# Kernel optimization log

Hardware: AMD Instinct MI355X
Metric: run time of the kernel (lower is better)

The kernel has to match this reference:

```python
import jax, jax.numpy as jnp
import numpy as np

DIM = 1024
HEADS = 16
DIM_HEAD = 64
INNER = HEADS * DIM_HEAD  # 1024
SCALE = DIM_HEAD ** -0.5


def setup_inputs() -> dict:
    key = jax.random.key(0)
    ks = jax.random.split(key, 5)
    B, N = 4, 2048
    x = jax.random.normal(ks[0], (B, N, DIM), dtype=jnp.float32)
    # torch Linear weights are [out, in]; store transposed [in, out] for x @ W
    s = 1.0 / np.sqrt(DIM)
    Wq = jax.random.uniform(ks[1], (DIM, INNER), minval=-s, maxval=s, dtype=jnp.float32)
    Wkv = jax.random.uniform(ks[2], (DIM, 2 * INNER), minval=-s, maxval=s, dtype=jnp.float32)
    so = 1.0 / np.sqrt(INNER)
    Wo = jax.random.uniform(ks[3], (INNER, DIM), minval=-so, maxval=so, dtype=jnp.float32)
    bo = jax.random.uniform(ks[4], (DIM,), minval=-so, maxval=so, dtype=jnp.float32)
    return {"x": x, "Wq": Wq, "Wkv": Wkv, "Wo": Wo, "bo": bo}


def reference(x, Wq, Wkv, Wo, bo):
    B, N, _ = x.shape
    q = x @ Wq                      # [B, N, INNER]
    kv = x @ Wkv                    # [B, N, 2*INNER]
    k, v = jnp.split(kv, 2, axis=-1)

    def split_heads(t):
        return t.reshape(B, N, HEADS, DIM_HEAD).transpose(0, 2, 1, 3)  # [B,H,N,D]

    q, k, v = split_heads(q) * SCALE, split_heads(k), split_heads(v)
    sim = jnp.einsum('bhid,bhjd->bhij', q, k)  # [B,H,N,N]
    mask_value = -jnp.finfo(sim.dtype).max
    # causal: mask strictly-upper triangle (triu with offset j-i+1 = 1)
    causal_mask = jnp.triu(jnp.ones((N, N), dtype=bool), k=1)
    sim = jnp.where(causal_mask[None, None, :, :], mask_value, sim)
    attn = jax.nn.softmax(sim, axis=-1)
    out = jnp.einsum('bhij,bhjd->bhid', attn, v)            # [B,H,N,D]
    out = out.transpose(0, 2, 1, 3).reshape(B, N, INNER)    # [B,N,INNER]
    return out @ Wo + bo
```

## Files before the change

kernel.cpp:

```cpp
#include <hip/hip_runtime.h>

typedef unsigned short u16;
typedef __bf16 bf16x8 __attribute__((ext_vector_type(8)));
typedef float floatx4 __attribute__((ext_vector_type(4)));
typedef unsigned as1_u32 __attribute__((address_space(1)));
typedef unsigned as3_u32 __attribute__((address_space(3)));

__device__ inline u16 f2bf(float f) {
    unsigned int u = __builtin_bit_cast(unsigned int, f);
    u += 0x7fffu + ((u >> 16) & 1u);
    return (u16)(u >> 16);
}
__device__ inline floatx4 mfma16(bf16x8 a, bf16x8 b, floatx4 c) {
    return __builtin_amdgcn_mfma_f32_16x16x32_bf16(a, b, c, 0, 0, 0);
}
__device__ inline void gld16(const u16* g, u16* l) {
    __builtin_amdgcn_global_load_lds((const as1_u32*)g, (as3_u32*)l, 16, 0, 0);
}
__device__ inline unsigned permpack(float lo, float hi) {
    return __builtin_amdgcn_perm(__builtin_bit_cast(unsigned, hi),
                                 __builtin_bit_cast(unsigned, lo), 0x07060302u);
}

#define NSEQ 2048
#define DIM  1024
#define HEADS 16
#define DHEAD 64
#define QSCALE 0.18033688f
#define CSHIFT 4.328085f

__global__ __launch_bounds__(256) void conv_x(const float* __restrict__ src,
                                              u16* __restrict__ dst) {
    const size_t i = ((size_t)blockIdx.x * 256 + threadIdx.x) * 8;
    float4 a = *(const float4*)&src[i];
    float4 b = *(const float4*)&src[i + 4];
    u16 o[8] __attribute__((aligned(16)));
    o[0] = f2bf(a.x); o[1] = f2bf(a.y); o[2] = f2bf(a.z); o[3] = f2bf(a.w);
    o[4] = f2bf(b.x); o[5] = f2bf(b.y); o[6] = f2bf(b.z); o[7] = f2bf(b.w);
    *(uint4*)&dst[i] = *(const uint4*)o;
}

__global__ __launch_bounds__(256) void transpose_conv(const float* __restrict__ src,
                                                      u16* __restrict__ dst, int ncols) {
    __shared__ u16 tile[64][72];
    const int n0 = blockIdx.x * 64, k0 = blockIdx.y * 64;
    const int t = threadIdx.x;
    #pragma unroll
    for (int rr = 0; rr < 4; rr++) {
        const int k = (t >> 4) + rr * 16;
        const int n = (t & 15) * 4;
        float4 v = *(const float4*)&src[(size_t)(k0 + k) * ncols + n0 + n];
        tile[n + 0][k] = f2bf(v.x); tile[n + 1][k] = f2bf(v.y);
        tile[n + 2][k] = f2bf(v.z); tile[n + 3][k] = f2bf(v.w);
    }
    __syncthreads();
    #pragma unroll
    for (int ww = 0; ww < 2; ww++) {
        const int idx = t + ww * 256;
        const int n = idx >> 3, g = idx & 7;
        u16 tmp[8] __attribute__((aligned(16)));
        #pragma unroll
        for (int i = 0; i < 8; i++) tmp[i] = tile[n][g * 8 + i];
        *(uint4*)&dst[(size_t)(n0 + n) * 1024 + k0 + g * 8] = *(const uint4*)tmp;
    }
}

__global__ __launch_bounds__(256) void qkv_gemm_v3(
    const u16* __restrict__ xb, const u16* __restrict__ Wt,
    u16* __restrict__ q_ws, u16* __restrict__ k_ws, u16* __restrict__ v_ws)
{
    __shared__ u16 a0[128 * 32], a1[128 * 32];
    __shared__ u16 b0[128 * 32], b1[128 * 32];

    const int n0 = blockIdx.x * 128;
    const int m0 = blockIdx.y * 128;
    const int t = threadIdx.x, lane = t & 63, w = t >> 6;
    const int wr = w >> 1, wc = w & 1;
    const int quad = lane >> 4, l16 = lane & 15;
    const int lrow = lane >> 2, lk = (lane & 3) * 8;

    floatx4 acc[4][4];
    #pragma unroll
    for (int i = 0; i < 4; i++)
        #pragma unroll
        for (int j = 0; j < 4; j++) acc[i][j] = floatx4{0.f, 0.f, 0.f, 0.f};

    for (int k0 = 0; k0 < DIM; k0 += 64) {
        __syncthreads();
        #pragma unroll
        for (int hh = 0; hh < 2; hh++) {
            const int row = w * 32 + hh * 16;
            const size_t ga = (size_t)(m0 + row + lrow) * DIM + k0 + lk;
            const size_t gb = (size_t)(n0 + row + lrow) * DIM + k0 + lk;
            gld16(&xb[ga],      &a0[row * 32]);
            gld16(&xb[ga + 32], &a1[row * 32]);
            gld16(&Wt[gb],      &b0[row * 32]);
            gld16(&Wt[gb + 32], &b1[row * 32]);
        }
        __syncthreads();

        #pragma unroll
        for (int ks = 0; ks < 2; ks++) {
            const u16* al = ks ? a1 : a0;
            const u16* bl = ks ? b1 : b0;
            bf16x8 af[4], bf[4];
            #pragma unroll
            for (int i = 0; i < 4; i++)
                af[i] = *(const bf16x8*)&al[(wr * 64 + i * 16 + l16) * 32 + quad * 8];
            #pragma unroll
            for (int j = 0; j < 4; j++)
                bf[j] = *(const bf16x8*)&bl[(wc * 64 + j * 16 + l16) * 32 + quad * 8];
            #pragma unroll
            for (int i = 0; i < 4; i++)
                #pragma unroll
                for (int j = 0; j < 4; j++)
                    acc[i][j] = mfma16(af[i], bf[j], acc[i][j]);
        }
    }

    const int seg = n0 >> 10;
    #pragma unroll
    for (int j = 0; j < 4; j++) {
        const int n  = n0 + wc * 64 + j * 16 + l16;
        const int nn = n & 1023;
        const int h  = nn >> 6, d = nn & 63;
        #pragma unroll
        for (int i = 0; i < 4; i++) {
            const int mb = m0 + wr * 64 + i * 16 + quad * 4;
            const int b = mb >> 11, ib = mb & (NSEQ - 1);
            if (seg == 0) {
                #pragma unroll
                for (int r = 0; r < 4; r++)
                    q_ws[(((size_t)(b * HEADS + h)) * NSEQ + ib + r) * DHEAD + d] =
                        f2bf(acc[i][j][r] * QSCALE);
            } else if (seg == 1) {
                #pragma unroll
                for (int r = 0; r < 4; r++)
                    k_ws[(((size_t)(b * HEADS + h)) * NSEQ + ib + r) * DHEAD + d] =
                        f2bf(acc[i][j][r]);
            } else {
                u16 tmp[4] __attribute__((aligned(8)));
                #pragma unroll
                for (int r = 0; r < 4; r++) tmp[r] = f2bf(acc[i][j][r]);
                *(uint2*)&v_ws[(((size_t)(b * HEADS + h)) * DHEAD + d) * NSEQ + ib] =
                    *(const uint2*)tmp;
            }
        }
    }
}

__global__ __launch_bounds__(256) void attn_v6(
    const u16* __restrict__ q_ws, const u16* __restrict__ k_ws,
    const u16* __restrict__ v_ws, u16* __restrict__ attn_ws)
{
    __shared__ u16 kds[2][64 * 64];
    __shared__ u16 vds[2][64 * 64];
    __shared__ u16 p_lds[4 * 32 * 72];

    const int bid = blockIdx.x;
    const int bh  = bid & 63;
    const int t16 = 15 - (bid >> 6);
    const int i0  = t16 * 128;
    const int b   = bh >> 4, h = bh & 15;

    const u16* qb = q_ws + (size_t)bh * NSEQ * DHEAD;
    const u16* kb = k_ws + (size_t)bh * NSEQ * DHEAD;
    const u16* vb = v_ws + (size_t)bh * DHEAD * NSEQ;

    const int t    = threadIdx.x;
    const int lane = t & 63, w = t >> 6;
    const int quad = lane >> 4, l16 = lane & 15;

    const int srow8 = lane >> 3;
    const int chunk = (lane & 7) ^ srow8;
    const int krow  = w * 16 + srow8;
    const size_t koff = (size_t)krow * DHEAD + chunk * 8;
    const size_t voff = (size_t)krow * NSEQ + chunk * 8;
    u16* klbase = (u16*)&kds[0][0] + w * 1024;
    u16* vlbase = (u16*)&vds[0][0] + w * 1024;

    bf16x8 qf[2][2];
    #pragma unroll
    for (int rf = 0; rf < 2; rf++)
        #pragma unroll
        for (int dg = 0; dg < 2; dg++)
            qf[rf][dg] = *(const bf16x8*)&qb[(size_t)(i0 + rf * 64 + w * 16 + l16) * DHEAD
                                             + dg * 32 + quad * 8];

    floatx4 l4[2] = {floatx4{0.f,0.f,0.f,0.f}, floatx4{0.f,0.f,0.f,0.f}};
    floatx4 acc[2][4];
    #pragma unroll
    for (int rf = 0; rf < 2; rf++)
        #pragma unroll
        for (int dg = 0; dg < 4; dg++) acc[rf][dg] = floatx4{0.f, 0.f, 0.f, 0.f};

    const int jt_max = 2 * t16 + 1;

    {
        gld16(&kb[koff],               klbase);
        gld16(&kb[koff + 8 * DHEAD],   klbase + 512);
        gld16(&vb[voff],               vlbase);
        gld16(&vb[voff + 8 * NSEQ],    vlbase + 512);
    }

    for (int jt = 0; jt <= jt_max; jt++) {
        const int cur = jt & 1;
        __syncthreads();

        if (jt < jt_max) {
            const size_t j64 = (size_t)(jt + 1) * 64;
            const int nb = (cur ^ 1) * 4096;
            gld16(&kb[j64 * DHEAD + koff],             klbase + nb);
            gld16(&kb[j64 * DHEAD + koff + 8 * DHEAD], klbase + nb + 512);
            gld16(&vb[j64 + voff],                     vlbase + nb);
            gld16(&vb[j64 + voff + 8 * NSEQ],          vlbase + nb + 512);
        }

        const u16* kl = &kds[cur][0];
        const u16* vl = &vds[cur][0];
        const int j0 = jt * 64;
        const int sw = (l16 & 7);

        floatx4 s[2][4];
        #pragma unroll
        for (int rf = 0; rf < 2; rf++)
            #pragma unroll
            for (int g = 0; g < 4; g++)
                s[rf][g] = floatx4{-CSHIFT, -CSHIFT, -CSHIFT, -CSHIFT};
        #pragma unroll
        for (int dg = 0; dg < 2; dg++)
            #pragma unroll
            for (int g = 0; g < 4; g++) {
                bf16x8 kf = *(const bf16x8*)&kl[(g * 16 + l16) * 64
                                                + (((dg * 4 + quad) ^ sw) * 8)];
                s[0][g] = mfma16(kf, qf[0][dg], s[0][g]);
                s[1][g] = mfma16(kf, qf[1][dg], s[1][g]);
            }

        #pragma unroll
        for (int rf = 0; rf < 2; rf++) {
            const int imin = i0 + rf * 64 + w * 16;
            if (j0 + 63 > imin) {
                const int i = imin + l16;
                #pragma unroll
                for (int g = 0; g < 4; g++) {
                    const int jb = j0 + g * 16 + quad * 4;
                    #pragma unroll
                    for (int r = 0; r < 4; r++)
                        if (jb + r > i) s[rf][g][r] = -1e30f;
                }
            }
        }

        #pragma unroll
        for (int rf = 0; rf < 2; rf++) {
            #pragma unroll
            for (int g = 0; g < 4; g++) {
                #pragma unroll
                for (int r = 0; r < 4; r++)
                    s[rf][g][r] = __builtin_amdgcn_exp2f(s[rf][g][r]);
                l4[rf] += s[rf][g];
                uint2 pk;
                pk.x = permpack(s[rf][g][0], s[rf][g][1]);
                pk.y = permpack(s[rf][g][2], s[rf][g][3]);
                *(uint2*)&p_lds[w * 2304 + (rf * 16 + l16) * 72 + g * 16 + quad * 4] = pk;
            }
        }
        asm volatile("s_waitcnt lgkmcnt(0)" ::: "memory");

        #pragma unroll
        for (int jg = 0; jg < 2; jg++) {
            bf16x8 pf0 = *(const bf16x8*)&p_lds[w * 2304 + l16 * 72 + jg * 32 + quad * 8];
            bf16x8 pf1 = *(const bf16x8*)&p_lds[w * 2304 + (16 + l16) * 72 + jg * 32 + quad * 8];
            #pragma unroll
            for (int dg = 0; dg < 4; dg++) {
                bf16x8 vf = *(const bf16x8*)&vl[(dg * 16 + l16) * 64
                                                + (((jg * 4 + quad) ^ sw) * 8)];
                acc[0][dg] = mfma16(pf0, vf, acc[0][dg]);
                acc[1][dg] = mfma16(pf1, vf, acc[1][dg]);
            }
        }
    }

    float l_ln[2];
    #pragma unroll
    for (int rf = 0; rf < 2; rf++) {
        l_ln[rf] = (l4[rf][0] + l4[rf][1]) + (l4[rf][2] + l4[rf][3]);
        l_ln[rf] += __shfl_xor(l_ln[rf], 16);
        l_ln[rf] += __shfl_xor(l_ln[rf], 32);
    }

    #pragma unroll
    for (int rf = 0; rf < 2; rf++) {
        float l_row[4];
        #pragma unroll
        for (int r = 0; r < 4; r++)
            l_row[r] = __shfl(l_ln[rf], quad * 4 + r);
        #pragma unroll
        for (int dg = 0; dg < 4; dg++)
            #pragma unroll
            for (int r = 0; r < 4; r++) {
                const float o = acc[rf][dg][r] / l_row[r];
                const int i = i0 + rf * 64 + w * 16 + quad * 4 + r;
                attn_ws[(((size_t)(b * NSEQ + i)) * HEADS + h) * DHEAD + dg * 16 + l16] = f2bf(o);
            }
    }
}

__global__ __launch_bounds__(256) void out_gemm_v3(
    const u16* __restrict__ attn, const u16* __restrict__ Wot,
    const float* __restrict__ bo, float* __restrict__ out)
{
    __shared__ u16 a0[128 * 32], a1[128 * 32];
    __shared__ u16 b0[128 * 32], b1[128 * 32];

    const int n0 = blockIdx.x * 128;
    const int m0 = blockIdx.y * 128;
    const int t = threadIdx.x, lane = t & 63, w = t >> 6;
    const int wr = w >> 1, wc = w & 1;
    const int quad = lane >> 4, l16 = lane & 15;
    const int lrow = lane >> 2, lk = (lane & 3) * 8;

    floatx4 acc[4][4];
    #pragma unroll
    for (int i = 0; i < 4; i++)
        #pragma unroll
        for (int j = 0; j < 4; j++) acc[i][j] = floatx4{0.f, 0.f, 0.f, 0.f};

    for (int k0 = 0; k0 < DIM; k0 += 64) {
        __syncthreads();
        #pragma unroll
        for (int hh = 0; hh < 2; hh++) {
            const int row = w * 32 + hh * 16;
            const size_t ga = (size_t)(m0 + row + lrow) * DIM + k0 + lk;
            const size_t gb = (size_t)(n0 + row + lrow) * DIM + k0 + lk;
            gld16(&attn[ga],      &a0[row * 32]);
            gld16(&attn[ga + 32], &a1[row * 32]);
            gld16(&Wot[gb],       &b0[row * 32]);
            gld16(&Wot[gb + 32],  &b1[row * 32]);
        }
        __syncthreads();

        #pragma unroll
        for (int ks = 0; ks < 2; ks++) {
            const u16* al = ks ? a1 : a0;
            const u16* bl = ks ? b1 : b0;
            bf16x8 af[4], bf[4];
            #pragma unroll
            for (int i = 0; i < 4; i++)
                af[i] = *(const bf16x8*)&al[(wr * 64 + i * 16 + l16) * 32 + quad * 8];
            #pragma unroll
            for (int j = 0; j < 4; j++)
                bf[j] = *(const bf16x8*)&bl[(wc * 64 + j * 16 + l16) * 32 + quad * 8];
            #pragma unroll
            for (int i = 0; i < 4; i++)
                #pragma unroll
                for (int j = 0; j < 4; j++)
                    acc[i][j] = mfma16(af[i], bf[j], acc[i][j]);
        }
    }

    #pragma unroll
    for (int j = 0; j < 4; j++) {
        const int n = n0 + wc * 64 + j * 16 + l16;
        const float bias = bo[n];
        #pragma unroll
        for (int i = 0; i < 4; i++) {
            #pragma unroll
            for (int r = 0; r < 4; r++) {
                const int m = m0 + wr * 64 + i * 16 + quad * 4 + r;
                out[(size_t)m * DIM + n] = acc[i][j][r] + bias;
            }
        }
    }
}

extern "C" void kernel_launch(void* const* d_in, const int* in_sizes, int n_in,
                              void* d_out, int out_size, void* d_ws, size_t ws_size,
                              hipStream_t stream) {
    const float* x   = (const float*)d_in[0];
    const float* Wq  = (const float*)d_in[1];
    const float* Wkv = (const float*)d_in[2];
    const float* Wo  = (const float*)d_in[3];
    const float* bo  = (const float*)d_in[4];

    u16* q_ws = (u16*)d_out;
    u16* xb   = (u16*)d_out + (size_t)8388608;

    u16* ws   = (u16*)d_ws;
    u16* k_ws = ws;
    u16* v_ws = ws + (size_t)8388608;
    u16* a_ws = ws + (size_t)16777216;
    u16* Wt   = a_ws;
    u16* Wot  = k_ws;

    conv_x<<<4096, 256, 0, stream>>>(x, xb);
    transpose_conv<<<dim3(16, 16), 256, 0, stream>>>(Wq, Wt, 1024);
    transpose_conv<<<dim3(32, 16), 256, 0, stream>>>(Wkv, Wt + (size_t)1024 * 1024, 2048);
    qkv_gemm_v3<<<dim3(24, 64), 256, 0, stream>>>(xb, Wt, q_ws, k_ws, v_ws);
    attn_v6<<<dim3(1024), 256, 0, stream>>>(q_ws, k_ws, v_ws, a_ws);
    transpose_conv<<<dim3(16, 16), 256, 0, stream>>>(Wo, Wot, 1024);
    out_gemm_v3<<<dim3(8, 64), 256, 0, stream>>>(a_ws, Wot, bo, (float*)d_out);
}
```

Baseline: 256.8 us.

## Enlarge QKV GEMM tile to 256x128 and pair causal attention tiles per block

The QKV GEMM now uses a 256x128 output tile with each wave owning 64 rows across all 128 columns, which doubles B-fragment reuse per wave and halves the grid. The attention kernel now processes two query tiles per block, a long one (15-pr) and a short one (pr), so every block does the same amount of causal work and the grid is 512 blocks. The GEMM change raises accumulator register use (4x8 floatx4) and may lower occupancy. Halving the attention grid reduces parallelism on a many-CU device.

```diff
diff --git a/kernel.cpp b/kernel.cpp
--- a/kernel.cpp
+++ b/kernel.cpp
@@ -65,35 +65,38 @@
     }
 }
 
-__global__ __launch_bounds__(256) void qkv_gemm_v3(
+__global__ __launch_bounds__(256) void qkv_gemm_v4(
     const u16* __restrict__ xb, const u16* __restrict__ Wt,
     u16* __restrict__ q_ws, u16* __restrict__ k_ws, u16* __restrict__ v_ws)
 {
-    __shared__ u16 a0[128 * 32], a1[128 * 32];
+    __shared__ u16 a0[256 * 32], a1[256 * 32];
     __shared__ u16 b0[128 * 32], b1[128 * 32];
 
     const int n0 = blockIdx.x * 128;
-    const int m0 = blockIdx.y * 128;
+    const int m0 = blockIdx.y * 256;
     const int t = threadIdx.x, lane = t & 63, w = t >> 6;
-    const int wr = w >> 1, wc = w & 1;
     const int quad = lane >> 4, l16 = lane & 15;
     const int lrow = lane >> 2, lk = (lane & 3) * 8;
 
-    floatx4 acc[4][4];
+    floatx4 acc[4][8];
     #pragma unroll
     for (int i = 0; i < 4; i++)
         #pragma unroll
-        for (int j = 0; j < 4; j++) acc[i][j] = floatx4{0.f, 0.f, 0.f, 0.f};
+        for (int j = 0; j < 8; j++) acc[i][j] = floatx4{0.f, 0.f, 0.f, 0.f};
 
     for (int k0 = 0; k0 < DIM; k0 += 64) {
         __syncthreads();
         #pragma unroll
+        for (int hh = 0; hh < 4; hh++) {
+            const int row = w * 64 + hh * 16;
+            const size_t ga = (size_t)(m0 + row + lrow) * DIM + k0 + lk;
+            gld16(&xb[ga],      &a0[row * 32]);
+            gld16(&xb[ga + 32], &a1[row * 32]);
+        }
+        #pragma unroll
         for (int hh = 0; hh < 2; hh++) {
             const int row = w * 32 + hh * 16;
-            const size_t ga = (size_t)(m0 + row + lrow) * DIM + k0 + lk;
             const size_t gb = (size_t)(n0 + row + lrow) * DIM + k0 + lk;
-            gld16(&xb[ga],      &a0[row * 32]);
-            gld16(&xb[ga + 32], &a1[row * 32]);
             gld16(&Wt[gb],      &b0[row * 32]);
             gld16(&Wt[gb + 32], &b1[row * 32]);
         }
@@ -103,30 +106,30 @@
         for (int ks = 0; ks < 2; ks++) {
             const u16* al = ks ? a1 : a0;
             const u16* bl = ks ? b1 : b0;
-            bf16x8 af[4], bf[4];
+            bf16x8 af[4], bf[8];
             #pragma unroll
             for (int i = 0; i < 4; i++)
-                af[i] = *(const bf16x8*)&al[(wr * 64 + i * 16 + l16) * 32 + quad * 8];
-            #pragma unroll
-            for (int j = 0; j < 4; j++)
-                bf[j] = *(const bf16x8*)&bl[(wc * 64 + j * 16 + l16) * 32 + quad * 8];
+                af[i] = *(const bf16x8*)&al[(w * 64 + i * 16 + l16) * 32 + quad * 8];
+            #pragma unroll
+            for (int j = 0; j < 8; j++)
+                bf[j] = *(const bf16x8*)&bl[(j * 16 + l16) * 32 + quad * 8];
             #pragma unroll
             for (int i = 0; i < 4; i++)
                 #pragma unroll
-                for (int j = 0; j < 4; j++)
+                for (int j = 0; j < 8; j++)
                     acc[i][j] = mfma16(af[i], bf[j], acc[i][j]);
         }
     }
 
     const int seg = n0 >> 10;
     #pragma unroll
-    for (int j = 0; j < 4; j++) {
-        const int n  = n0 + wc * 64 + j * 16 + l16;
+    for (int j = 0; j < 8; j++) {
+        const int n  = n0 + j * 16 + l16;
         const int nn = n & 1023;
         const int h  = nn >> 6, d = nn & 63;
         #pragma unroll
         for (int i = 0; i < 4; i++) {
-            const int mb = m0 + wr * 64 + i * 16 + quad * 4;
+            const int mb = m0 + w * 64 + i * 16 + quad * 4;
             const int b = mb >> 11, ib = mb & (NSEQ - 1);
             if (seg == 0) {
                 #pragma unroll
@@ -149,7 +152,7 @@
     }
 }
 
-__global__ __launch_bounds__(256) void attn_v6(
+__global__ __launch_bounds__(256) void attn_v7(
     const u16* __restrict__ q_ws, const u16* __restrict__ k_ws,
     const u16* __restrict__ v_ws, u16* __restrict__ attn_ws)
 {
@@ -159,8 +162,7 @@
 
     const int bid = blockIdx.x;
     const int bh  = bid & 63;
-    const int t16 = 15 - (bid >> 6);
-    const int i0  = t16 * 128;
+    const int pr  = bid >> 6;
     const int b   = bh >> 4, h = bh & 15;
 
     const u16* qb = q_ws + (size_t)bh * NSEQ * DHEAD;
@@ -178,132 +180,130 @@
     const size_t voff = (size_t)krow * NSEQ + chunk * 8;
     u16* klbase = (u16*)&kds[0][0] + w * 1024;
     u16* vlbase = (u16*)&vds[0][0] + w * 1024;
-
-    bf16x8 qf[2][2];
-    #pragma unroll
-    for (int rf = 0; rf < 2; rf++)
-        #pragma unroll
-        for (int dg = 0; dg < 2; dg++)
-            qf[rf][dg] = *(const bf16x8*)&qb[(size_t)(i0 + rf * 64 + w * 16 + l16) * DHEAD
-                                             + dg * 32 + quad * 8];
-
-    floatx4 l4[2] = {floatx4{0.f,0.f,0.f,0.f}, floatx4{0.f,0.f,0.f,0.f}};
-    floatx4 acc[2][4];
-    #pragma unroll
-    for (int rf = 0; rf < 2; rf++)
-        #pragma unroll
-        for (int dg = 0; dg < 4; dg++) acc[rf][dg] = floatx4{0.f, 0.f, 0.f, 0.f};
-
-    const int jt_max = 2 * t16 + 1;
-
-    {
-        gld16(&kb[koff],               klbase);
-        gld16(&kb[koff + 8 * DHEAD],   klbase + 512);
-        gld16(&vb[voff],               vlbase);
-        gld16(&vb[voff + 8 * NSEQ],    vlbase + 512);
-    }
-
-    for (int jt = 0; jt <= jt_max; jt++) {
-        const int cur = jt & 1;
-        __syncthreads();
-
-        if (jt < jt_max) {
-            const size_t j64 = (size_t)(jt + 1) * 64;
-            const int nb = (cur ^ 1) * 4096;
-            gld16(&kb[j64 * DHEAD + koff],             klbase + nb);
-            gld16(&kb[j64 * DHEAD + koff + 8 * DHEAD], klbase + nb + 512);
-            gld16(&vb[j64 + voff],                     vlbase + nb);
-            gld16(&vb[j64 + voff + 8 * NSEQ],          vlbase + nb + 512);
-        }
-
-        const u16* kl = &kds[cur][0];
-        const u16* vl = &vds[cur][0];
-        const int j0 = jt * 64;
-        const int sw = (l16 & 7);
-
-        floatx4 s[2][4];
+    const int sw = (l16 & 7);
+
+    for (int ph = 0; ph < 2; ph++) {
+        const int t16 = ph ? pr : (15 - pr);
+        const int i0  = t16 * 128;
+        const int jt_max = 2 * t16 + 1;
+
+        bf16x8 qf[2][2];
         #pragma unroll
         for (int rf = 0; rf < 2; rf++)
             #pragma unroll
-            for (int g = 0; g < 4; g++)
-                s[rf][g] = floatx4{-CSHIFT, -CSHIFT, -CSHIFT, -CSHIFT};
-        #pragma unroll
-        for (int dg = 0; dg < 2; dg++)
-            #pragma unroll
-            for (int g = 0; g < 4; g++) {
-                bf16x8 kf = *(const bf16x8*)&kl[(g * 16 + l16) * 64
-                                                + (((dg * 4 + quad) ^ sw) * 8)];
-                s[0][g] = mfma16(kf, qf[0][dg], s[0][g]);
-                s[1][g] = mfma16(kf, qf[1][dg], s[1][g]);
-            }
-
-        #pragma unroll
-        for (int rf = 0; rf < 2; rf++) {
-            const int imin = i0 + rf * 64 + w * 16;
-            if (j0 + 63 > imin) {
-                const int i = imin + l16;
+            for (int dg = 0; dg < 2; dg++)
+                qf[rf][dg] = *(const bf16x8*)&qb[(size_t)(i0 + rf * 64 + w * 16 + l16) * DHEAD
+                                                 + dg * 32 + quad * 8];
+
+        floatx4 l4[2] = {floatx4{0.f,0.f,0.f,0.f}, floatx4{0.f,0.f,0.f,0.f}};
+        floatx4 acc[2][4];
+        #pragma unroll
+        for (int rf = 0; rf < 2; rf++)
+            #pragma unroll
+            for (int dg = 0; dg < 4; dg++) acc[rf][dg] = floatx4{0.f, 0.f, 0.f, 0.f};
+
+        gld16(&kb[koff],             klbase);
+        gld16(&kb[koff + 8 * DHEAD], klbase + 512);
+        gld16(&vb[voff],             vlbase);
+        gld16(&vb[voff + 8 * NSEQ],  vlbase + 512);
+
+        for (int jt = 0; jt <= jt_max; jt++) {
+            const int cur = jt & 1;
+            __syncthreads();
+
+            if (jt < jt_max) {
+                const size_t j64 = (size_t)(jt + 1) * 64;
+                const int nb = (cur ^ 1) * 4096;
+                gld16(&kb[j64 * DHEAD + koff],             klbase + nb);
+                gld16(&kb[j64 * DHEAD + koff + 8 * DHEAD], klbase + nb + 512);
+                gld16(&vb[j64 + voff],                     vlbase + nb);
+                gld16(&vb[j64 + voff + 8 * NSEQ],          vlbase + nb + 512);
+            }
+
+            const u16* kl = &kds[cur][0];
+            const u16* vl = &vds[cur][0];
+            const int j0 = jt * 64;
+
+            floatx4 s[2][4];
+            #pragma unroll
+            for (int rf = 0; rf < 2; rf++)
+                #pragma unroll
+                for (int g = 0; g < 4; g++)
+                    s[rf][g] = floatx4{-CSHIFT, -CSHIFT, -CSHIFT, -CSHIFT};
+            #pragma unroll
+            for (int dg = 0; dg < 2; dg++)
                 #pragma unroll
                 for (int g = 0; g < 4; g++) {
-                    const int jb = j0 + g * 16 + quad * 4;
+                    bf16x8 kf = *(const bf16x8*)&kl[(g * 16 + l16) * 64
+                                                    + (((dg * 4 + quad) ^ sw) * 8)];
+                    s[0][g] = mfma16(kf, qf[0][dg], s[0][g]);
+                    s[1][g] = mfma16(kf, qf[1][dg], s[1][g]);
+                }
+
+            #pragma unroll
+            for (int rf = 0; rf < 2; rf++) {
+                const int imin = i0 + rf * 64 + w * 16;
+                if (j0 + 63 > imin) {
+                    const int i = imin + l16;
+                    #pragma unroll
+                    for (int g = 0; g < 4; g++) {
+                        const int jb = j0 + g * 16 + quad * 4;
+                        #pragma unroll
+                        for (int r = 0; r < 4; r++)
+                            if (jb + r > i) s[rf][g][r] = -1e30f;
+                    }
+                }
+            }
+
+            #pragma unroll
+            for (int rf = 0; rf < 2; rf++) {
+                #pragma unroll
+                for (int g = 0; g < 4; g++) {
                     #pragma unroll
                     for (int r = 0; r < 4; r++)
-                        if (jb + r > i) s[rf][g][r] = -1e30f;
+                        s[rf][g][r] = __builtin_amdgcn_exp2f(s[rf][g][r]);
+                    l4[rf] += s[rf][g];
+                    uint2 pk;
+                    pk.x = permpack(s[rf][g][0], s[rf][g][1]);
+                    pk.y = permpack(s[rf][g][2], s[rf][g][3]);
+                    *(uint2*)&p_lds[w * 2304 + (rf * 16 + l16) * 72 + g * 16 + quad * 4] = pk;
                 }
             }
+            asm volatile("s_waitcnt lgkmcnt(0)" ::: "memory");
+
+            #pragma unroll
+            for (int jg = 0; jg < 2; jg++) {
+                bf16x8 pf0 = *(const bf16x8*)&p_lds[w * 2304 + l16 * 72 + jg * 32 + quad * 8];
+                bf16x8 pf1 = *(const bf16x8*)&p_lds[w * 2304 + (16 + l16) * 72 + jg * 32 + quad * 8];
+                #pragma unroll
+                for (int dg = 0; dg < 4; dg++) {
+                    bf16x8 vf = *(const bf16x8*)&vl[(dg * 16 + l16) * 64
+                                                    + (((jg * 4 + quad) ^ sw) * 8)];
+                    acc[0][dg] = mfma16(pf0, vf, acc[0][dg]);
+                    acc[1][dg] = mfma16(pf1, vf, acc[1][dg]);
+                }
+            }
         }
 
         #pragma unroll
         for (int rf = 0; rf < 2; rf++) {
-            #pragma unroll
-            for (int g = 0; g < 4; g++) {
-                #pragma unroll
-                for (int r = 0; r < 4; r++)
-                    s[rf][g][r] = __builtin_amdgcn_exp2f(s[rf][g][r]);
-                l4[rf] += s[rf][g];
-                uint2 pk;
-                pk.x = permpack(s[rf][g][0], s[rf][g][1]);
-                pk.y = permpack(s[rf][g][2], s[rf][g][3]);
-                *(uint2*)&p_lds[w * 2304 + (rf * 16 + l16) * 72 + g * 16 + quad * 4] = pk;
-            }
-        }
-        asm volatile("s_waitcnt lgkmcnt(0)" ::: "memory");
-
-        #pragma unroll
-        for (int jg = 0; jg < 2; jg++) {
-            bf16x8 pf0 = *(const bf16x8*)&p_lds[w * 2304 + l16 * 72 + jg * 32 + quad * 8];
-            bf16x8 pf1 = *(const bf16x8*)&p_lds[w * 2304 + (16 + l16) * 72 + jg * 32 + quad * 8];
-            #pragma unroll
-            for (int dg = 0; dg < 4; dg++) {
-                bf16x8 vf = *(const bf16x8*)&vl[(dg * 16 + l16) * 64
-                                                + (((jg * 4 + quad) ^ sw) * 8)];
-                acc[0][dg] = mfma16(pf0, vf, acc[0][dg]);
-                acc[1][dg] = mfma16(pf1, vf, acc[1][dg]);
-            }
-        }
-    }
-
-    float l_ln[2];
-    #pragma unroll
-    for (int rf = 0; rf < 2; rf++) {
-        l_ln[rf] = (l4[rf][0] + l4[rf][1]) + (l4[rf][2] + l4[rf][3]);
-        l_ln[rf] += __shfl_xor(l_ln[rf], 16);
-        l_ln[rf] += __shfl_xor(l_ln[rf], 32);
-    }
-
-    #pragma unroll
-    for (int rf = 0; rf < 2; rf++) {
-        float l_row[4];
-        #pragma unroll
-        for (int r = 0; r < 4; r++)
-            l_row[r] = __shfl(l_ln[rf], quad * 4 + r);
-        #pragma unroll
-        for (int dg = 0; dg < 4; dg++)
-            #pragma unroll
-            for (int r = 0; r < 4; r++) {
-                const float o = acc[rf][dg][r] / l_row[r];
-                const int i = i0 + rf * 64 + w * 16 + quad * 4 + r;
-                attn_ws[(((size_t)(b * NSEQ + i)) * HEADS + h) * DHEAD + dg * 16 + l16] = f2bf(o);
-            }
+            float l_ln = (l4[rf][0] + l4[rf][1]) + (l4[rf][2] + l4[rf][3]);
+            l_ln += __shfl_xor(l_ln, 16);
+            l_ln += __shfl_xor(l_ln, 32);
+            float l_row[4];
+            #pragma unroll
+            for (int r = 0; r < 4; r++)
+                l_row[r] = __shfl(l_ln, quad * 4 + r);
+            #pragma unroll
+            for (int dg = 0; dg < 4; dg++)
+                #pragma unroll
+                for (int r = 0; r < 4; r++) {
+                    const float o = acc[rf][dg][r] / l_row[r];
+                    const int i = i0 + rf * 64 + w * 16 + quad * 4 + r;
+                    attn_ws[(((size_t)(b * NSEQ + i)) * HEADS + h) * DHEAD + dg * 16 + l16] =
+                        f2bf(o);
+                }
+        }
     }
 }
 
@@ -397,8 +397,8 @@
     conv_x<<<4096, 256, 0, stream>>>(x, xb);
     transpose_conv<<<dim3(16, 16), 256, 0, stream>>>(Wq, Wt, 1024);
     transpose_conv<<<dim3(32, 16), 256, 0, stream>>>(Wkv, Wt + (size_t)1024 * 1024, 2048);
-    qkv_gemm_v3<<<dim3(24, 64), 256, 0, stream>>>(xb, Wt, q_ws, k_ws, v_ws);
-    attn_v6<<<dim3(1024), 256, 0, stream>>>(q_ws, k_ws, v_ws, a_ws);
+    qkv_gemm_v4<<<dim3(24, 32), 256, 0, stream>>>(xb, Wt, q_ws, k_ws, v_ws);
+    attn_v7<<<dim3(512), 256, 0, stream>>>(q_ws, k_ws, v_ws, a_ws);
     transpose_conv<<<dim3(16, 16), 256, 0, stream>>>(Wo, Wot, 1024);
     out_gemm_v3<<<dim3(8, 64), 256, 0, stream>>>(a_ws, Wot, bo, (float*)d_out);
 }
```

New measurement: 294.9 us. 1.15x slower.

## Pair causal query tiles per attention block and fuse prep kernels

Applied to the files above, without the earlier changes.

The attention kernel now runs 512 blocks, and each block handles two 128-row query tiles: tile 15-pr and tile pr. Every block therefore covers the same total number of causal key tiles, which balances work and removes the tail of uneven block lengths. The x conversion and the Wq/Wkv transpose-convert kernels are merged into a single launch to cut launch overhead. The trade-off is fewer blocks in flight for attention, which may lower occupancy and latency hiding on a GPU with many CUs.

```diff
diff --git a/kernel.cpp b/kernel.cpp
--- a/kernel.cpp
+++ b/kernel.cpp
@@ -29,22 +29,10 @@
 #define QSCALE 0.18033688f
 #define CSHIFT 4.328085f
 
-__global__ __launch_bounds__(256) void conv_x(const float* __restrict__ src,
-                                              u16* __restrict__ dst) {
-    const size_t i = ((size_t)blockIdx.x * 256 + threadIdx.x) * 8;
-    float4 a = *(const float4*)&src[i];
-    float4 b = *(const float4*)&src[i + 4];
-    u16 o[8] __attribute__((aligned(16)));
-    o[0] = f2bf(a.x); o[1] = f2bf(a.y); o[2] = f2bf(a.z); o[3] = f2bf(a.w);
-    o[4] = f2bf(b.x); o[5] = f2bf(b.y); o[6] = f2bf(b.z); o[7] = f2bf(b.w);
-    *(uint4*)&dst[i] = *(const uint4*)o;
-}
-
-__global__ __launch_bounds__(256) void transpose_conv(const float* __restrict__ src,
-                                                      u16* __restrict__ dst, int ncols) {
+__device__ inline void transpose_tile(const float* __restrict__ src,
+                                      u16* __restrict__ dst, int ncols,
+                                      int n0, int k0, int t) {
     __shared__ u16 tile[64][72];
-    const int n0 = blockIdx.x * 64, k0 = blockIdx.y * 64;
-    const int t = threadIdx.x;
     #pragma unroll
     for (int rr = 0; rr < 4; rr++) {
         const int k = (t >> 4) + rr * 16;
@@ -63,6 +51,35 @@
         for (int i = 0; i < 8; i++) tmp[i] = tile[n][g * 8 + i];
         *(uint4*)&dst[(size_t)(n0 + n) * 1024 + k0 + g * 8] = *(const uint4*)tmp;
     }
+}
+
+__global__ __launch_bounds__(256) void prep_fused(
+    const float* __restrict__ x,  u16* __restrict__ xb,
+    const float* __restrict__ Wq, const float* __restrict__ Wkv,
+    u16* __restrict__ Wt)
+{
+    const int bid = blockIdx.x;
+    const int t = threadIdx.x;
+    if (bid < 4096) {
+        const size_t i = ((size_t)bid * 256 + t) * 8;
+        float4 a = *(const float4*)&x[i];
+        float4 b = *(const float4*)&x[i + 4];
+        u16 o[8] __attribute__((aligned(16)));
+        o[0] = f2bf(a.x); o[1] = f2bf(a.y); o[2] = f2bf(a.z); o[3] = f2bf(a.w);
+        o[4] = f2bf(b.x); o[5] = f2bf(b.y); o[6] = f2bf(b.z); o[7] = f2bf(b.w);
+        *(uint4*)&xb[i] = *(const uint4*)o;
+    } else if (bid < 4352) {
+        const int v = bid - 4096;
+        transpose_tile(Wq, Wt, 1024, (v & 15) * 64, (v >> 4) * 64, t);
+    } else {
+        const int v = bid - 4352;
+        transpose_tile(Wkv, Wt + (size_t)1024 * 1024, 2048, (v & 31) * 64, (v >> 5) * 64, t);
+    }
+}
+
+__global__ __launch_bounds__(256) void transpose_conv(const float* __restrict__ src,
+                                                      u16* __restrict__ dst, int ncols) {
+    transpose_tile(src, dst, ncols, blockIdx.x * 64, blockIdx.y * 64, threadIdx.x);
 }
 
 __global__ __launch_bounds__(256) void qkv_gemm_v3(
@@ -149,7 +166,7 @@
     }
 }
 
-__global__ __launch_bounds__(256) void attn_v6(
+__global__ __launch_bounds__(256) void attn_v7(
     const u16* __restrict__ q_ws, const u16* __restrict__ k_ws,
     const u16* __restrict__ v_ws, u16* __restrict__ attn_ws)
 {
@@ -159,8 +176,7 @@
 
     const int bid = blockIdx.x;
     const int bh  = bid & 63;
-    const int t16 = 15 - (bid >> 6);
-    const int i0  = t16 * 128;
+    const int pr  = bid >> 6;
     const int b   = bh >> 4, h = bh & 15;
 
     const u16* qb = q_ws + (size_t)bh * NSEQ * DHEAD;
@@ -178,132 +194,130 @@
     const size_t voff = (size_t)krow * NSEQ + chunk * 8;
     u16* klbase = (u16*)&kds[0][0] + w * 1024;
     u16* vlbase = (u16*)&vds[0][0] + w * 1024;
-
-    bf16x8 qf[2][2];
-    #pragma unroll
-    for (int rf = 0; rf < 2; rf++)
-        #pragma unroll
-        for (int dg = 0; dg < 2; dg++)
-            qf[rf][dg] = *(const bf16x8*)&qb[(size_t)(i0 + rf * 64 + w * 16 + l16) * DHEAD
-                                             + dg * 32 + quad * 8];
-
-    floatx4 l4[2] = {floatx4{0.f,0.f,0.f,0.f}, floatx4{0.f,0.f,0.f,0.f}};
-    floatx4 acc[2][4];
-    #pragma unroll
-    for (int rf = 0; rf < 2; rf++)
-        #pragma unroll
-        for (int dg = 0; dg < 4; dg++) acc[rf][dg] = floatx4{0.f, 0.f, 0.f, 0.f};
-
-    const int jt_max = 2 * t16 + 1;
-
-    {
-        gld16(&kb[koff],               klbase);
-        gld16(&kb[koff + 8 * DHEAD],   klbase + 512);
-        gld16(&vb[voff],               vlbase);
-        gld16(&vb[voff + 8 * NSEQ],    vlbase + 512);
-    }
-
-    for (int jt = 0; jt <= jt_max; jt++) {
-        const int cur = jt & 1;
-        __syncthreads();
-
-        if (jt < jt_max) {
-            const size_t j64 = (size_t)(jt + 1) * 64;
-            const int nb = (cur ^ 1) * 4096;
-            gld16(&kb[j64 * DHEAD + koff],             klbase + nb);
-            gld16(&kb[j64 * DHEAD + koff + 8 * DHEAD], klbase + nb + 512);
-            gld16(&vb[j64 + voff],                     vlbase + nb);
-            gld16(&vb[j64 + voff + 8 * NSEQ],          vlbase + nb + 512);
-        }
-
-        const u16* kl = &kds[cur][0];
-        const u16* vl = &vds[cur][0];
-        const int j0 = jt * 64;
-        const int sw = (l16 & 7);
-
-        floatx4 s[2][4];
+    const int sw = (l16 & 7);
+
+    for (int ph = 0; ph < 2; ph++) {
+        const int t16 = ph ? pr : (15 - pr);
+        const int i0  = t16 * 128;
+        const int jt_max = 2 * t16 + 1;
+
+        bf16x8 qf[2][2];
         #pragma unroll
         for (int rf = 0; rf < 2; rf++)
             #pragma unroll
-            for (int g = 0; g < 4; g++)
-                s[rf][g] = floatx4{-CSHIFT, -CSHIFT, -CSHIFT, -CSHIFT};
-        #pragma unroll
-        for (int dg = 0; dg < 2; dg++)
-            #pragma unroll
-            for (int g = 0; g < 4; g++) {
-                bf16x8 kf = *(const bf16x8*)&kl[(g * 16 + l16) * 64
-                                                + (((dg * 4 + quad) ^ sw) * 8)];
-                s[0][g] = mfma16(kf, qf[0][dg], s[0][g]);
-                s[1][g] = mfma16(kf, qf[1][dg], s[1][g]);
-            }
-
-        #pragma unroll
-        for (int rf = 0; rf < 2; rf++) {
-            const int imin = i0 + rf * 64 + w * 16;
-            if (j0 + 63 > imin) {
-                const int i = imin + l16;
+            for (int dg = 0; dg < 2; dg++)
+                qf[rf][dg] = *(const bf16x8*)&qb[(size_t)(i0 + rf * 64 + w * 16 + l16) * DHEAD
+                                                 + dg * 32 + quad * 8];
+
+        floatx4 l4[2] = {floatx4{0.f,0.f,0.f,0.f}, floatx4{0.f,0.f,0.f,0.f}};
+        floatx4 acc[2][4];
+        #pragma unroll
+        for (int rf = 0; rf < 2; rf++)
+            #pragma unroll
+            for (int dg = 0; dg < 4; dg++) acc[rf][dg] = floatx4{0.f, 0.f, 0.f, 0.f};
+
+        gld16(&kb[koff],             klbase);
+        gld16(&kb[koff + 8 * DHEAD], klbase + 512);
+        gld16(&vb[voff],             vlbase);
+        gld16(&vb[voff + 8 * NSEQ],  vlbase + 512);
+
+        for (int jt = 0; jt <= jt_max; jt++) {
+            const int cur = jt & 1;
+            __syncthreads();
+
+            if (jt < jt_max) {
+                const size_t j64 = (size_t)(jt + 1) * 64;
+                const int nb = (cur ^ 1) * 4096;
+                gld16(&kb[j64 * DHEAD + koff],             klbase + nb);
+                gld16(&kb[j64 * DHEAD + koff + 8 * DHEAD], klbase + nb + 512);
+                gld16(&vb[j64 + voff],                     vlbase + nb);
+                gld16(&vb[j64 + voff + 8 * NSEQ],          vlbase + nb + 512);
+            }
+
+            const u16* kl = &kds[cur][0];
+            const u16* vl = &vds[cur][0];
+            const int j0 = jt * 64;
+
+            floatx4 s[2][4];
+            #pragma unroll
+            for (int rf = 0; rf < 2; rf++)
+                #pragma unroll
+                for (int g = 0; g < 4; g++)
+                    s[rf][g] = floatx4{-CSHIFT, -CSHIFT, -CSHIFT, -CSHIFT};
+            #pragma unroll
+            for (int dg = 0; dg < 2; dg++)
                 #pragma unroll
                 for (int g = 0; g < 4; g++) {
-                    const int jb = j0 + g * 16 + quad * 4;
+                    bf16x8 kf = *(const bf16x8*)&kl[(g * 16 + l16) * 64
+                                                    + (((dg * 4 + quad) ^ sw) * 8)];
+                    s[0][g] = mfma16(kf, qf[0][dg], s[0][g]);
+                    s[1][g] = mfma16(kf, qf[1][dg], s[1][g]);
+                }
+
+            #pragma unroll
+            for (int rf = 0; rf < 2; rf++) {
+                const int imin = i0 + rf * 64 + w * 16;
+                if (j0 + 63 > imin) {
+                    const int i = imin + l16;
+                    #pragma unroll
+                    for (int g = 0; g < 4; g++) {
+                        const int jb = j0 + g * 16 + quad * 4;
+                        #pragma unroll
+                        for (int r = 0; r < 4; r++)
+                            if (jb + r > i) s[rf][g][r] = -1e30f;
+                    }
+                }
+            }
+
+            #pragma unroll
+            for (int rf = 0; rf < 2; rf++) {
+                #pragma unroll
+                for (int g = 0; g < 4; g++) {
                     #pragma unroll
                     for (int r = 0; r < 4; r++)
-                        if (jb + r > i) s[rf][g][r] = -1e30f;
+                        s[rf][g][r] = __builtin_amdgcn_exp2f(s[rf][g][r]);
+                    l4[rf] += s[rf][g];
+                    uint2 pk;
+                    pk.x = permpack(s[rf][g][0], s[rf][g][1]);
+                    pk.y = permpack(s[rf][g][2], s[rf][g][3]);
+                    *(uint2*)&p_lds[w * 2304 + (rf * 16 + l16) * 72 + g * 16 + quad * 4] = pk;
                 }
             }
+            asm volatile("s_waitcnt lgkmcnt(0)" ::: "memory");
+
+            #pragma unroll
+            for (int jg = 0; jg < 2; jg++) {
+                bf16x8 pf0 = *(const bf16x8*)&p_lds[w * 2304 + l16 * 72 + jg * 32 + quad * 8];
+                bf16x8 pf1 = *(const bf16x8*)&p_lds[w * 2304 + (16 + l16) * 72 + jg * 32 + quad * 8];
+                #pragma unroll
+                for (int dg = 0; dg < 4; dg++) {
+                    bf16x8 vf = *(const bf16x8*)&vl[(dg * 16 + l16) * 64
+                                                    + (((jg * 4 + quad) ^ sw) * 8)];
+                    acc[0][dg] = mfma16(pf0, vf, acc[0][dg]);
+                    acc[1][dg] = mfma16(pf1, vf, acc[1][dg]);
+                }
+            }
         }
 
         #pragma unroll
         for (int rf = 0; rf < 2; rf++) {
-            #pragma unroll
-            for (int g = 0; g < 4; g++) {
-                #pragma unroll
-                for (int r = 0; r < 4; r++)
-                    s[rf][g][r] = __builtin_amdgcn_exp2f(s[rf][g][r]);
-                l4[rf] += s[rf][g];
-                uint2 pk;
-                pk.x = permpack(s[rf][g][0], s[rf][g][1]);
-                pk.y = permpack(s[rf][g][2], s[rf][g][3]);
-                *(uint2*)&p_lds[w * 2304 + (rf * 16 + l16) * 72 + g * 16 + quad * 4] = pk;
-            }
-        }
-        asm volatile("s_waitcnt lgkmcnt(0)" ::: "memory");
-
-        #pragma unroll
-        for (int jg = 0; jg < 2; jg++) {
-            bf16x8 pf0 = *(const bf16x8*)&p_lds[w * 2304 + l16 * 72 + jg * 32 + quad * 8];
-            bf16x8 pf1 = *(const bf16x8*)&p_lds[w * 2304 + (16 + l16) * 72 + jg * 32 + quad * 8];
-            #pragma unroll
-            for (int dg = 0; dg < 4; dg++) {
-                bf16x8 vf = *(const bf16x8*)&vl[(dg * 16 + l16) * 64
-                                                + (((jg * 4 + quad) ^ sw) * 8)];
-                acc[0][dg] = mfma16(pf0, vf, acc[0][dg]);
-                acc[1][dg] = mfma16(pf1, vf, acc[1][dg]);
-            }
-        }
-    }
-
-    float l_ln[2];
-    #pragma unroll
-    for (int rf = 0; rf < 2; rf++) {
-        l_ln[rf] = (l4[rf][0] + l4[rf][1]) + (l4[rf][2] + l4[rf][3]);
-        l_ln[rf] += __shfl_xor(l_ln[rf], 16);
-        l_ln[rf] += __shfl_xor(l_ln[rf], 32);
-    }
-
-    #pragma unroll
-    for (int rf = 0; rf < 2; rf++) {
-        float l_row[4];
-        #pragma unroll
-        for (int r = 0; r < 4; r++)
-            l_row[r] = __shfl(l_ln[rf], quad * 4 + r);
-        #pragma unroll
-        for (int dg = 0; dg < 4; dg++)
-            #pragma unroll
-            for (int r = 0; r < 4; r++) {
-                const float o = acc[rf][dg][r] / l_row[r];
-                const int i = i0 + rf * 64 + w * 16 + quad * 4 + r;
-                attn_ws[(((size_t)(b * NSEQ + i)) * HEADS + h) * DHEAD + dg * 16 + l16] = f2bf(o);
-            }
+            float l_ln = (l4[rf][0] + l4[rf][1]) + (l4[rf][2] + l4[rf][3]);
+            l_ln += __shfl_xor(l_ln, 16);
+            l_ln += __shfl_xor(l_ln, 32);
+            float l_row[4];
+            #pragma unroll
+            for (int r = 0; r < 4; r++)
+                l_row[r] = __shfl(l_ln, quad * 4 + r);
+            #pragma unroll
+            for (int dg = 0; dg < 4; dg++)
+                #pragma unroll
+                for (int r = 0; r < 4; r++) {
+                    const float o = acc[rf][dg][r] / l_row[r];
+                    const int i = i0 + rf * 64 + w * 16 + quad * 4 + r;
+                    attn_ws[(((size_t)(b * NSEQ + i)) * HEADS + h) * DHEAD + dg * 16 + l16] =
+                        f2bf(o);
+                }
+        }
     }
 }
 
@@ -394,11 +408,9 @@
     u16* Wt   = a_ws;
     u16* Wot  = k_ws;
 
-    conv_x<<<4096, 256, 0, stream>>>(x, xb);
-    transpose_conv<<<dim3(16, 16), 256, 0, stream>>>(Wq, Wt, 1024);
-    transpose_conv<<<dim3(32, 16), 256, 0, stream>>>(Wkv, Wt + (size_t)1024 * 1024, 2048);
+    prep_fused<<<4864, 256, 0, stream>>>(x, xb, Wq, Wkv, Wt);
     qkv_gemm_v3<<<dim3(24, 64), 256, 0, stream>>>(xb, Wt, q_ws, k_ws, v_ws);
-    attn_v6<<<dim3(1024), 256, 0, stream>>>(q_ws, k_ws, v_ws, a_ws);
+    attn_v7<<<dim3(512), 256, 0, stream>>>(q_ws, k_ws, v_ws, a_ws);
     transpose_conv<<<dim3(16, 16), 256, 0, stream>>>(Wo, Wot, 1024);
     out_gemm_v3<<<dim3(8, 64), 256, 0, stream>>>(a_ws, Wot, bo, (float*)d_out);
 }
```

Result: no change. 259.2 us (+0.9%).
